# Optimization experiments

Measured on AMD Instinct MI355X. Metric: run time of the kernel, lower is better.

The kernel has to match this reference:

```python
import jax, jax.numpy as jnp
import numpy as np

MARGIN = 1.0

def setup_inputs() -> dict:
    key = jax.random.key(0)
    k1, k2 = jax.random.split(key)
    B, C = 65536, 1000
    pred = jax.random.normal(k1, (B, C), dtype=jnp.float32)
    target = jax.random.randint(k2, (B,), 0, C, dtype=jnp.int64)
    return {"pred": pred, "target": target}

def reference(pred, target):
    # pred: [B, C], target: [B]
    B, C = pred.shape
    correct = jnp.take_along_axis(pred, target[:, None], axis=1)  # [B, 1]
    margins = pred - correct + MARGIN                              # [B, C]
    # exclude the true class (its margin would be exactly MARGIN)
    is_target = jnp.arange(C)[None, :] == target[:, None]
    margins = jnp.where(is_target, -jnp.inf, margins)
    # per-sample hinge: max(0, max_{j != y} margins)
    per_sample = jnp.maximum(jnp.max(margins, axis=1), 0.0)        # [B]
    return jnp.mean(per_sample)
```

## Files before the change

kernel.cpp:

```cpp
#include <hip/hip_runtime.h>
#include <hip/hip_bf16.h>
#include <math.h>

#define BLOCK 256
#define WAVES_PER_BLOCK (BLOCK / 64)
#define GRID1 2048

typedef float f32x4 __attribute__((ext_vector_type(4)));

__global__ __launch_bounds__(BLOCK) void hinge_rows_kernel(
    const float* __restrict__ pred, const int* __restrict__ target,
    float* __restrict__ partial, int B, int C) {
  const int lane = threadIdx.x & 63;
  const int wave = threadIdx.x >> 6;
  const int gwave = blockIdx.x * WAVES_PER_BLOCK + wave;
  const int nwaves = gridDim.x * WAVES_PER_BLOCK;
  const int rpw = (B + nwaves - 1) / nwaves;
  const int base = gwave * rpw;
  const int nvec = C >> 2;

  int ty = 0;
  float corr = 0.0f;
  if (lane < rpw && base + lane < B) {
    ty = target[base + lane];
    corr = pred[(size_t)(base + lane) * (size_t)C + ty];
  }

  float sum = 0.0f;

  for (int k = 0; k < rpw; ++k) {
    const int row = base + k;
    if (row >= B) break;
    const int y = __shfl(ty, k);
    const float correct = __shfl(corr, k);

    const float* rp = pred + (size_t)row * (size_t)C;
    const f32x4* rp4 = (const f32x4*)rp;

    float m = -INFINITY;
    #pragma unroll 4
    for (int i = lane; i < nvec; i += 64) {
      f32x4 v = __builtin_nontemporal_load(&rp4[i]);
      const int b0 = i << 2;
      v.x = (b0 + 0 == y) ? -INFINITY : v.x;
      v.y = (b0 + 1 == y) ? -INFINITY : v.y;
      v.z = (b0 + 2 == y) ? -INFINITY : v.z;
      v.w = (b0 + 3 == y) ? -INFINITY : v.w;
      m = fmaxf(m, fmaxf(fmaxf(v.x, v.y), fmaxf(v.z, v.w)));
    }
    for (int c = (nvec << 2) + lane; c < C; c += 64) {
      if (c != y) m = fmaxf(m, rp[c]);
    }

    #pragma unroll
    for (int off = 32; off; off >>= 1)
      m = fmaxf(m, __shfl_xor(m, off));

    sum += fmaxf(m - correct + 1.0f, 0.0f);
  }

  __shared__ float lsum[WAVES_PER_BLOCK];
  if (lane == 0) lsum[wave] = sum;
  __syncthreads();
  if (threadIdx.x == 0) {
    float s = 0.0f;
    #pragma unroll
    for (int w = 0; w < WAVES_PER_BLOCK; ++w) s += lsum[w];
    partial[blockIdx.x] = s;
  }
}

__global__ __launch_bounds__(BLOCK) void hinge_reduce_kernel(
    const float* __restrict__ partial, int n, float* __restrict__ out,
    float scale) {
  float s = 0.0f;
  for (int i = threadIdx.x; i < n; i += BLOCK) s += partial[i];

  #pragma unroll
  for (int off = 32; off; off >>= 1) s += __shfl_xor(s, off);

  const int lane = threadIdx.x & 63;
  const int wave = threadIdx.x >> 6;
  __shared__ float lsum[WAVES_PER_BLOCK];
  if (lane == 0) lsum[wave] = s;
  __syncthreads();
  if (threadIdx.x == 0) {
    float t = 0.0f;
    #pragma unroll
    for (int w = 0; w < WAVES_PER_BLOCK; ++w) t += lsum[w];
    out[0] = t * scale;
  }
}

extern "C" void kernel_launch(void* const* d_in, const int* in_sizes, int n_in,
                              void* d_out, int out_size, void* d_ws, size_t ws_size,
                              hipStream_t stream) {
  const float* pred = (const float*)d_in[0];
  const int* target = (const int*)d_in[1];
  float* out = (float*)d_out;
  float* partial = (float*)d_ws;

  const int B = in_sizes[1];
  const int C = in_sizes[0] / B;

  hinge_rows_kernel<<<GRID1, BLOCK, 0, stream>>>(pred, target, partial, B, C);
  hinge_reduce_kernel<<<1, BLOCK, 0, stream>>>(partial, GRID1, out, 1.0f / (float)B);
}
```

Baseline: 349.9 us.

## Process eight rows per wave with eight lanes per row

Each wave now handles eight rows at once, eight lanes per row, using a grid-stride loop over row groups. This replaces the old scheme, where all 64 lanes walked one row at a time and paid a full 64-lane shuffle reduction per row. Per-row max reductions shrink to three shuffles, and the hinge terms are summed across the eight rows with shuffles. Each row's reads are now split into separate 128-byte segments rather than wide contiguous accesses, and the nontemporal load hint is dropped.

```diff
diff --git a/kernel.cpp b/kernel.cpp
--- a/kernel.cpp
+++ b/kernel.cpp
@@ -13,34 +13,33 @@
     float* __restrict__ partial, int B, int C) {
   const int lane = threadIdx.x & 63;
   const int wave = threadIdx.x >> 6;
+  const int g = lane & 7;
+  const int r = lane >> 3;
   const int gwave = blockIdx.x * WAVES_PER_BLOCK + wave;
   const int nwaves = gridDim.x * WAVES_PER_BLOCK;
-  const int rpw = (B + nwaves - 1) / nwaves;
-  const int base = gwave * rpw;
   const int nvec = C >> 2;
-
-  int ty = 0;
-  float corr = 0.0f;
-  if (lane < rpw && base + lane < B) {
-    ty = target[base + lane];
-    corr = pred[(size_t)(base + lane) * (size_t)C + ty];
-  }
 
   float sum = 0.0f;
 
-  for (int k = 0; k < rpw; ++k) {
-    const int row = base + k;
-    if (row >= B) break;
-    const int y = __shfl(ty, k);
-    const float correct = __shfl(corr, k);
+  for (int base = gwave * 8; base < B; base += nwaves * 8) {
+    int ty = 0;
+    float corr = 0.0f;
+    const bool own = (lane < 8) && (base + lane < B);
+    if (own) {
+      ty = target[base + lane];
+      corr = pred[(size_t)(base + lane) * (size_t)C + ty];
+    }
 
-    const float* rp = pred + (size_t)row * (size_t)C;
+    const int row = base + r;
+    const int rowv = (row < B) ? row : (B - 1);
+    const int y = __shfl(ty, r);
+    const float* rp = pred + (size_t)rowv * (size_t)C;
     const f32x4* rp4 = (const f32x4*)rp;
 
     float m = -INFINITY;
     #pragma unroll 4
-    for (int i = lane; i < nvec; i += 64) {
-      f32x4 v = __builtin_nontemporal_load(&rp4[i]);
+    for (int i = g; i < nvec; i += 8) {
+      f32x4 v = rp4[i];
       const int b0 = i << 2;
       v.x = (b0 + 0 == y) ? -INFINITY : v.x;
       v.y = (b0 + 1 == y) ? -INFINITY : v.y;
@@ -48,15 +47,21 @@
       v.w = (b0 + 3 == y) ? -INFINITY : v.w;
       m = fmaxf(m, fmaxf(fmaxf(v.x, v.y), fmaxf(v.z, v.w)));
     }
-    for (int c = (nvec << 2) + lane; c < C; c += 64) {
+    for (int c = (nvec << 2) + g; c < C; c += 8) {
       if (c != y) m = fmaxf(m, rp[c]);
     }
 
-    #pragma unroll
-    for (int off = 32; off; off >>= 1)
-      m = fmaxf(m, __shfl_xor(m, off));
+    m = fmaxf(m, __shfl_xor(m, 1));
+    m = fmaxf(m, __shfl_xor(m, 2));
+    m = fmaxf(m, __shfl_xor(m, 4));
 
-    sum += fmaxf(m - correct + 1.0f, 0.0f);
+    const float M = __shfl(m, (lane & 7) * 8);
+    float h = fmaxf(M - corr + 1.0f, 0.0f);
+    h = own ? h : 0.0f;
+    h += __shfl_xor(h, 1);
+    h += __shfl_xor(h, 2);
+    h += __shfl_xor(h, 4);
+    sum += h;
   }
 
   __shared__ float lsum[WAVES_PER_BLOCK];
```

Result: slower. 357.9 us (+2.3%).
